# Kernel tuning notes

Measured on AMD Instinct MI355X. Metric: run time of the kernel, lower is better.

Reference implementation:

```python
import jax, jax.numpy as jnp
import numpy as np

HIDDEN = 1024
QDIM = 16
B, S = 4, 2048
EPS = 1e-8


def setup_inputs() -> dict:
    key = jax.random.key(0)
    ks = jax.random.split(key, 12)
    sc_h = 1.0 / np.sqrt(HIDDEN)
    inp = {
        "x": jax.random.normal(ks[0], (B, S, HIDDEN), dtype=jnp.float32),
        "Wq": jax.random.normal(ks[1], (HIDDEN, HIDDEN), dtype=jnp.float32) * sc_h,
        "bq": jnp.zeros((HIDDEN,), dtype=jnp.float32),
        "Wk": jax.random.normal(ks[2], (HIDDEN, HIDDEN), dtype=jnp.float32) * sc_h,
        "bk": jnp.zeros((HIDDEN,), dtype=jnp.float32),
        "Wv": jax.random.normal(ks[3], (HIDDEN, HIDDEN), dtype=jnp.float32) * sc_h,
        "bv": jnp.zeros((HIDDEN,), dtype=jnp.float32),
        "We": jax.random.normal(ks[4], (HIDDEN, QDIM), dtype=jnp.float32) * sc_h,
        "be": jnp.zeros((QDIM,), dtype=jnp.float32),
        "Wo": jax.random.normal(ks[5], (HIDDEN, HIDDEN), dtype=jnp.float32) * sc_h,
        "bo": jnp.zeros((HIDDEN,), dtype=jnp.float32),
    }
    return inp


def _quantum_embed(h, We, be):
    # Linear projection to quantum amplitude space, then normalize to a unit state.
    z = h @ We + be                     # [..., QDIM]
    nrm = jnp.sqrt(jnp.sum(z * z, axis=-1, keepdims=True) + EPS)
    return z / nrm


def reference(x, Wq, bq, Wk, bk, Wv, bv, We, be, Wo, bo):
    # Projections
    q = x @ Wq + bq                     # [B,S,H]
    k = x @ Wk + bk
    v = x @ Wv + bv
    # Quantum state embeddings (unit-normalized amplitudes)
    q_q = _quantum_embed(q, We, be)     # [B,S,QDIM]
    k_q = _quantum_embed(k, We, be)
    # Quantum fidelity similarity |<q|k>|^2, vectorized over all pairs
    ov = jnp.einsum("bqd,bkd->bqk", q_q, k_q)   # [B,S,S]
    attn = jax.nn.softmax(ov * ov, axis=-1)
    attended = jnp.einsum("bqk,bkh->bqh", attn, v)
    return attended @ Wo + bo
```

## Files before the change

kernel.cpp:

```cpp
#include <hip/hip_runtime.h>

#define H 1024
#define QD 16
#define BATCH 4
#define SEQ 2048
#define MROWS 8192
#define KCH 64

typedef __bf16 bf16x8 __attribute__((ext_vector_type(8)));
typedef __bf16 bf16x4 __attribute__((ext_vector_type(4)));
typedef float f32x4 __attribute__((ext_vector_type(4)));

__device__ __forceinline__ void async_g2l_16(const void* g, void* l) {
  __builtin_amdgcn_global_load_lds(
      (const __attribute__((address_space(1))) unsigned int*)g,
      (__attribute__((address_space(3))) unsigned int*)l, 16, 0, 0);
}

__global__ __launch_bounds__(256) void cvt_split(const float* __restrict__ src,
                                                 __bf16* __restrict__ hi,
                                                 __bf16* __restrict__ lo, int n) {
  int i = (blockIdx.x * 256 + threadIdx.x) * 4;
  if (i < n) {
    float4 f = *(const float4*)(src + i);
    bf16x4 h, l;
    h[0] = (__bf16)f.x; l[0] = (__bf16)(f.x - (float)h[0]);
    h[1] = (__bf16)f.y; l[1] = (__bf16)(f.y - (float)h[1]);
    h[2] = (__bf16)f.z; l[2] = (__bf16)(f.z - (float)h[2]);
    h[3] = (__bf16)f.w; l[3] = (__bf16)(f.w - (float)h[3]);
    *(bf16x4*)(hi + i) = h;
    *(bf16x4*)(lo + i) = l;
  }
}

__global__ __launch_bounds__(256) void transpose_cvt_f32_bf16(
    const float* __restrict__ src, __bf16* __restrict__ dst, int R, int C) {
  __shared__ float t[32][33];
  const int rb = blockIdx.y * 32, cb = blockIdx.x * 32;
  const int c = threadIdx.x & 31;
  const int r0 = threadIdx.x >> 5;
#pragma unroll
  for (int rr = r0; rr < 32; rr += 8)
    t[rr][c] = src[(long)(rb + rr) * C + cb + c];
  __syncthreads();
#pragma unroll
  for (int rr = r0; rr < 32; rr += 8)
    dst[(long)(cb + rr) * R + rb + c] = (__bf16)t[c][rr];
}

__global__ __launch_bounds__(256) void k2_cqk(const float* __restrict__ Wq,
                                              const float* __restrict__ Wk,
                                              const float* __restrict__ We,
                                              __bf16* __restrict__ Cth,
                                              __bf16* __restrict__ Ctl) {
  const int gw = blockIdx.x * 4 + (threadIdx.x >> 6);
  const int lane = threadIdx.x & 63;
  const int mat = gw & 1, k = gw >> 1;
  const float* Wrow = (mat ? Wk : Wq) + (long)k * H;
  const int col = lane & 15, q4 = lane >> 4;
  const float* wp = Wrow + q4 * 256;
  const float* wep = We + (long)q4 * 256 * QD + col;
  float acc = 0.f;
#pragma unroll 4
  for (int n0 = 0; n0 < 256; n0 += 4) {
    float4 w4 = *(const float4*)(wp + n0);
    acc += w4.x * wep[(n0 + 0) * QD];
    acc += w4.y * wep[(n0 + 1) * QD];
    acc += w4.z * wep[(n0 + 2) * QD];
    acc += w4.w * wep[(n0 + 3) * QD];
  }
  acc += __shfl_xor(acc, 16);
  acc += __shfl_xor(acc, 32);
  if (lane < 16) {
    __bf16 hi = (__bf16)acc;
    __bf16 lo = (__bf16)(acc - (float)hi);
    long idx = (long)(mat * 16 + col) * H + k;
    Cth[idx] = hi;
    Ctl[idx] = lo;
  }
}

__global__ __launch_bounds__(512) void k2b_dvec(
    const float* __restrict__ bq, const float* __restrict__ bk,
    const float* __restrict__ We, const float* __restrict__ be,
    float* __restrict__ dvec) {
  __shared__ float part[16][32];
  const int tid = threadIdx.x;
  const int j = tid & 31, p = tid >> 5;
  const int mat = j >> 4, col = j & 15;
  const float* b = mat ? bk : bq;
  float acc = 0.f;
  for (int n = p * 64; n < p * 64 + 64; ++n) acc += b[n] * We[n * QD + col];
  part[p][j] = acc;
  __syncthreads();
  if (tid < 32) {
    float sum = be[tid & 15];
    for (int p2 = 0; p2 < 16; ++p2) sum += part[p2][tid];
    dvec[tid] = sum;
  }
}

__global__ __launch_bounds__(1024) void k3_embed_mfma(
    const __bf16* __restrict__ xh, const __bf16* __restrict__ xl,
    const __bf16* __restrict__ Cth, const __bf16* __restrict__ Ctl,
    const float* __restrict__ dvec, __bf16* __restrict__ qq32,
    __bf16* __restrict__ kk32) {
  __shared__ __bf16 Ah[4][32 * 64];
  __shared__ __bf16 Al[4][32 * 64];
  __shared__ __bf16 Bh[4][32 * 64];
  __shared__ __bf16 Bl[4][32 * 64];
  const int tid = threadIdx.x;
  const int lane = tid & 63;
  const int w = tid >> 6;
  const int kb = w >> 2;
  const int w4 = w & 3;
  const int rowhalf = w4 >> 1;
  const int ntile = w4 & 1;
  const int l15 = lane & 15, quad = lane >> 4;
  const long rowBase = (long)blockIdx.x * 32;

  const int half = tid >> 8;
  const int tl = tid & 255;
  const int srow = tl >> 3;
  const int seg = tl & 7;
  const int segsw = (seg ^ (srow & 7)) * 8;
  const long gk = half * 256 + segsw;
  const __bf16* agh = xh + (rowBase + srow) * H + gk;
  const __bf16* agl = xl + (rowBase + srow) * H + gk;
  const __bf16* bgh = Cth + (long)srow * H + gk;
  const __bf16* bgl = Ctl + (long)srow * H + gk;
  __bf16* lah = &Ah[half][srow * 64 + seg * 8];
  __bf16* lal = &Al[half][srow * 64 + seg * 8];
  __bf16* lbh = &Bh[half][srow * 64 + seg * 8];
  __bf16* lbl = &Bl[half][srow * 64 + seg * 8];

  f32x4 acc;
  acc[0] = 0.f; acc[1] = 0.f; acc[2] = 0.f; acc[3] = 0.f;
  const int arow = (rowhalf * 16 + l15) * 64;
  const int brow = (ntile * 16 + l15) * 64;
  const int h7 = l15 & 7;

  for (int k0 = 0; k0 < 256; k0 += 64) {
    async_g2l_16(agh + k0, lah);
    async_g2l_16(agl + k0, lal);
    async_g2l_16(bgh + k0, lbh);
    async_g2l_16(bgl + k0, lbl);
    __syncthreads();
#pragma unroll
    for (int s = 0; s < 2; ++s) {
      const int slot = ((s * 4 + quad) ^ h7) * 8;
      bf16x8 fah = *(const bf16x8*)&Ah[kb][arow + slot];
      bf16x8 fal = *(const bf16x8*)&Al[kb][arow + slot];
      bf16x8 fbh = *(const bf16x8*)&Bh[kb][brow + slot];
      bf16x8 fbl = *(const bf16x8*)&Bl[kb][brow + slot];
      acc = __builtin_amdgcn_mfma_f32_16x16x32_bf16(fah, fbh, acc, 0, 0, 0);
      acc = __builtin_amdgcn_mfma_f32_16x16x32_bf16(fal, fbh, acc, 0, 0, 0);
      acc = __builtin_amdgcn_mfma_f32_16x16x32_bf16(fah, fbl, acc, 0, 0, 0);
    }
    __syncthreads();
  }

  if (kb > 0) ((f32x4*)&Ah[kb][0])[w4 * 64 + lane] = acc;
  __syncthreads();
  if (kb == 0) {
#pragma unroll
    for (int q = 1; q < 4; ++q) {
      f32x4 o = ((const f32x4*)&Ah[q][0])[w4 * 64 + lane];
      acc[0] += o[0]; acc[1] += o[1]; acc[2] += o[2]; acc[3] += o[3];
    }
    const float dv = dvec[ntile * 16 + l15];
    const float osc = ntile ? 1.0f : 1.20112240878f;
    __bf16* outp = ntile ? kk32 : qq32;
#pragma unroll
    for (int r = 0; r < 4; ++r) {
      float z = acc[r] + dv;
      float s2 = z * z;
      s2 += __shfl_xor(s2, 1);
      s2 += __shfl_xor(s2, 2);
      s2 += __shfl_xor(s2, 4);
      s2 += __shfl_xor(s2, 8);
      float val = z * rsqrtf(s2 + 1e-8f) * osc;
      long row = rowBase + rowhalf * 16 + quad * 4 + r;
      outp[row * 32 + l15] = (__bf16)val;
      outp[row * 32 + 16 + l15] = (__bf16)0.f;
    }
  }
}

__global__ __launch_bounds__(1024) void fused_attn(
    const __bf16* __restrict__ qq32, const __bf16* __restrict__ kk32,
    const __bf16* __restrict__ v_t, __bf16* __restrict__ attn) {
  __shared__ __bf16 Vlds[3][256 * KCH];
  __shared__ __bf16 Plds[2][128 * KCH];
  __shared__ float rsum2[128 * 2];
  const int tid = threadIdx.x;
  const int lane = tid & 63;
  const int w = tid >> 6;
  const int l15 = lane & 15, quad = lane >> 4;
  const int sq = w >> 1, sk = w & 1;
  const int wp_h = w & 3, wp_q = w >> 2;

  const int bid = blockIdx.x;
  const int xcd = bid & 7, s = bid >> 3;
  const int panel = xcd * 2 + (s >> 4);
  const int b = panel >> 2;
  const long hbase = (long)(panel & 3) * 256;
  const long qbase = (long)(s & 15) * 128;

  const bf16x8 bq = *(const bf16x8*)(qq32 +
      ((long)b * SEQ + qbase + sq * 16 + l15) * 32 + quad * 8);
  const __bf16* kkb = kk32 + ((long)b * SEQ + sk * 32 + l15) * 32 + quad * 8;

  const int vR = tid >> 3;
  const int vSL = (tid & 7) ^ (vR & 7);
  const __bf16* vg0 = v_t + (long)b * H * SEQ + (hbase + vR) * SEQ + vSL * 8;
  const __bf16* vg1 = vg0 + (long)128 * SEQ;

  f32x4 acc[2][4];
#pragma unroll
  for (int i = 0; i < 2; ++i)
#pragma unroll
    for (int j = 0; j < 4; ++j) {
      acc[i][j][0] = 0.f; acc[i][j][1] = 0.f; acc[i][j][2] = 0.f; acc[i][j][3] = 0.f;
    }
  float rsPart = 0.f;

  async_g2l_16(vg0, &Vlds[0][vR * KCH + (tid & 7) * 8]);
  async_g2l_16(vg1, &Vlds[0][(vR + 128) * KCH + (tid & 7) * 8]);
  bf16x8 ak[2];
  ak[0] = *(const bf16x8*)kkb;
  ak[1] = *(const bf16x8*)(kkb + 16 * 32);

  int vcur = 0, vnxt = 1;
  for (int t = 0; t < SEQ / KCH; ++t) {
    const int kn = ((t + 1) & (SEQ / KCH - 1)) * KCH;
    async_g2l_16(vg0 + kn, &Vlds[vnxt][vR * KCH + (tid & 7) * 8]);
    async_g2l_16(vg1 + kn, &Vlds[vnxt][(vR + 128) * KCH + (tid & 7) * 8]);

    __bf16* Pw = Plds[t & 1];
#pragma unroll
    for (int i = 0; i < 2; ++i) {
      f32x4 s2v;
      s2v[0] = 0.f; s2v[1] = 0.f; s2v[2] = 0.f; s2v[3] = 0.f;
      s2v = __builtin_amdgcn_mfma_f32_16x16x32_bf16(ak[i], bq, s2v, 0, 0, 0);
      bf16x4 pw;
      float part = 0.f;
#pragma unroll
      for (int r = 0; r < 4; ++r) {
        float wgt = exp2f(s2v[r] * s2v[r]);
        part += wgt;
        pw[r] = (__bf16)wgt;
      }
      rsPart += part;
      const int q = sq * 16 + l15;
      const int g = sk * 4 + i * 2 + (quad >> 1);
      *(bf16x4*)&Pw[q * KCH + ((g ^ (q & 7)) << 3) + (quad & 1) * 4] = pw;
    }
    ak[0] = *(const bf16x8*)(kkb + (long)kn * 32);
    ak[1] = *(const bf16x8*)(kkb + (long)(kn + 16) * 32);

    asm volatile("s_waitcnt lgkmcnt(0)" ::: "memory");
    asm volatile("s_waitcnt vmcnt(4)" ::: "memory");
    __builtin_amdgcn_sched_barrier(0);
    __builtin_amdgcn_s_barrier();

    const __bf16* Vr = Vlds[vcur];
#pragma unroll
    for (int ks = 0; ks < 2; ++ks) {
      bf16x8 ap[2], bv[4];
#pragma unroll
      for (int i = 0; i < 2; ++i) {
        const int q = wp_q * 32 + i * 16 + l15;
        ap[i] = *(const bf16x8*)&Pw[q * KCH + (((ks * 4 + quad) ^ (q & 7)) << 3)];
      }
#pragma unroll
      for (int j = 0; j < 4; ++j) {
        const int vr = wp_h * 64 + j * 16 + l15;
        bv[j] = *(const bf16x8*)&Vr[vr * KCH + (((ks * 4 + quad) ^ (vr & 7)) << 3)];
      }
#pragma unroll
      for (int i = 0; i < 2; ++i)
#pragma unroll
        for (int j = 0; j < 4; ++j)
          acc[i][j] =
              __builtin_amdgcn_mfma_f32_16x16x32_bf16(ap[i], bv[j], acc[i][j], 0, 0, 0);
    }
    const int third = 3 - vcur - vnxt;
    vcur = vnxt;
    vnxt = third;
  }

  {
    float vs = rsPart;
    vs += __shfl_xor(vs, 16);
    vs += __shfl_xor(vs, 32);
    if (lane < 16) rsum2[(sq * 16 + l15) * 2 + sk] = vs;
  }
  __syncthreads();

  float rinv[2][4];
#pragma unroll
  for (int i = 0; i < 2; ++i)
#pragma unroll
    for (int r = 0; r < 4; ++r) {
      int row = wp_q * 32 + i * 16 + quad * 4 + r;
      rinv[i][r] = 1.0f / (rsum2[row * 2] + rsum2[row * 2 + 1]);
    }

  __bf16* ob = attn + ((long)b * SEQ + qbase) * H + hbase;
#pragma unroll
  for (int i = 0; i < 2; ++i)
#pragma unroll
    for (int j = 0; j < 4; ++j) {
      const int colL = wp_h * 64 + j * 16 + l15;
#pragma unroll
      for (int r = 0; r < 4; ++r) {
        const int rowL = wp_q * 32 + i * 16 + quad * 4 + r;
        ob[(long)rowL * H + colL] = (__bf16)(acc[i][j][r] * rinv[i][r]);
      }
    }
}

template <int OUTMODE, int HASBIAS>
__global__ __launch_bounds__(256) void gemm_bt(
    const __bf16* __restrict__ A, const __bf16* __restrict__ Bt,
    void* __restrict__ Cout, const float* __restrict__ bias, int M, int N, int K) {
  __shared__ __bf16 Alds[128 * 64];
  __shared__ __bf16 Blds[128 * 64];
  const int tid = threadIdx.x;
  const int lane = tid & 63;
  const int w = tid >> 6;
  const int wm = w >> 1, wn = w & 1;
  const int l15 = lane & 15, quad = lane >> 4;

  const int flat = blockIdx.y * 8 + blockIdx.x;
  const int xcd = flat & 7, idx = flat >> 3;
  const int rowPanel = xcd * 8 + (idx >> 3);
  const int colBlk = idx & 7;
  const long rowBase = (long)rowPanel * 128;
  const long colBase = (long)colBlk * 128;

  const int srow = lane >> 3;
  const int segsw = ((lane & 7) ^ srow) * 8;

  const __bf16* ag[4];
  const __bf16* bg[4];
  __bf16* as_[4];
  __bf16* bs_[4];
#pragma unroll
  for (int j = 0; j < 4; ++j) {
    int r = j * 32 + w * 8;
    ag[j] = A + (rowBase + r + srow) * (long)K + segsw;
    bg[j] = Bt + (colBase + r + srow) * (long)K + segsw;
    as_[j] = &Alds[r * 64 + (lane & 7) * 8];
    bs_[j] = &Blds[r * 64 + (lane & 7) * 8];
  }

  f32x4 acc[4][4];
#pragma unroll
  for (int i = 0; i < 4; ++i)
#pragma unroll
    for (int j = 0; j < 4; ++j) {
      acc[i][j][0] = 0.f; acc[i][j][1] = 0.f; acc[i][j][2] = 0.f; acc[i][j][3] = 0.f;
    }

  const int h7 = l15 & 7;

  for (int k0 = 0; k0 < K; k0 += 64) {
#pragma unroll
    for (int j = 0; j < 4; ++j) {
      async_g2l_16(ag[j], as_[j]);
      async_g2l_16(bg[j], bs_[j]);
      ag[j] += 64;
      bg[j] += 64;
    }
    __syncthreads();
#pragma unroll
    for (int s = 0; s < 2; ++s) {
      const int slot = ((s * 4 + quad) ^ h7) * 8;
      bf16x8 af[4], bfv[4];
#pragma unroll
      for (int i = 0; i < 4; ++i) {
        af[i] = *(const bf16x8*)&Alds[(wm * 64 + i * 16 + l15) * 64 + slot];
        bfv[i] = *(const bf16x8*)&Blds[(wn * 64 + i * 16 + l15) * 64 + slot];
      }
#pragma unroll
      for (int i = 0; i < 4; ++i)
#pragma unroll
        for (int j = 0; j < 4; ++j)
          acc[i][j] =
              __builtin_amdgcn_mfma_f32_16x16x32_bf16(af[i], bfv[j], acc[i][j], 0, 0, 0);
    }
    __syncthreads();
  }

  const long crow0 = rowBase + wm * 64 + quad * 4;
  const long ccol0 = colBase + wn * 64 + l15;
#pragma unroll
  for (int i = 0; i < 4; ++i) {
#pragma unroll
    for (int j = 0; j < 4; ++j) {
      long col = ccol0 + j * 16;
      float bb = HASBIAS ? bias[col] : 0.f;
      if (OUTMODE == 2) {
        long row0 = crow0 + i * 16;
        int bz = (int)(row0 >> 11);
        long rb = row0 & (SEQ - 1);
        bf16x4 pv;
#pragma unroll
        for (int r = 0; r < 4; ++r) pv[r] = (__bf16)(acc[i][j][r] + bb);
        *(bf16x4*)&((__bf16*)Cout)[((long)bz * N + col) * SEQ + rb] = pv;
      } else {
#pragma unroll
        for (int r = 0; r < 4; ++r) {
          long row = crow0 + i * 16 + r;
          float val = acc[i][j][r] + bb;
          if (OUTMODE == 0)
            ((float*)Cout)[row * N + col] = val;
          else
            ((__bf16*)Cout)[row * N + col] = (__bf16)val;
        }
      }
    }
  }
}

extern "C" void kernel_launch(void* const* d_in, const int* in_sizes, int n_in,
                              void* d_out, int out_size, void* d_ws, size_t ws_size,
                              hipStream_t stream) {
  const float* x = (const float*)d_in[0];
  const float* Wq = (const float*)d_in[1];
  const float* bq = (const float*)d_in[2];
  const float* Wk = (const float*)d_in[3];
  const float* bk = (const float*)d_in[4];
  const float* Wv = (const float*)d_in[5];
  const float* bv = (const float*)d_in[6];
  const float* We = (const float*)d_in[7];
  const float* be = (const float*)d_in[8];
  const float* Wo = (const float*)d_in[9];
  const float* bo = (const float*)d_in[10];
  float* out = (float*)d_out;

  char* ws = (char*)d_ws;
  size_t o = 0;
  auto alloc = [&](size_t n) {
    size_t r = o;
    o += (n + 255) & ~(size_t)255;
    return r;
  };
  __bf16* xbf = (__bf16*)(ws + alloc((size_t)MROWS * H * 2));
  __bf16* v_t = (__bf16*)(ws + alloc((size_t)MROWS * H * 2));
  __bf16* attn = (__bf16*)(ws + alloc((size_t)MROWS * H * 2));
  __bf16* Wvt = (__bf16*)(ws + alloc((size_t)H * H * 2));
  __bf16* Wot = (__bf16*)(ws + alloc((size_t)H * H * 2));
  __bf16* Cth = (__bf16*)(ws + alloc((size_t)32 * H * 2));
  __bf16* Ctl = (__bf16*)(ws + alloc((size_t)32 * H * 2));
  float* dvec = (float*)(ws + alloc(32 * 4));
  __bf16* qq32 = (__bf16*)(ws + alloc((size_t)MROWS * 32 * 2));
  __bf16* kk32 = (__bf16*)(ws + alloc((size_t)MROWS * 32 * 2));
  __bf16* xlo = attn;
  if (ws_size < o) return;

  cvt_split<<<MROWS * H / 1024, 256, 0, stream>>>(x, xbf, xlo, MROWS * H);
  transpose_cvt_f32_bf16<<<dim3(32, 32), 256, 0, stream>>>(Wv, Wvt, H, H);
  transpose_cvt_f32_bf16<<<dim3(32, 32), 256, 0, stream>>>(Wo, Wot, H, H);
  k2_cqk<<<512, 256, 0, stream>>>(Wq, Wk, We, Cth, Ctl);
  k2b_dvec<<<1, 512, 0, stream>>>(bq, bk, We, be, dvec);
  k3_embed_mfma<<<MROWS / 32, 1024, 0, stream>>>(xbf, xlo, Cth, Ctl, dvec, qq32, kk32);
  gemm_bt<2, 1><<<dim3(8, 64), 256, 0, stream>>>(xbf, Wvt, v_t, bv, MROWS, H, H);
  fused_attn<<<256, 1024, 0, stream>>>(qq32, kk32, v_t, attn);
  gemm_bt<0, 1><<<dim3(8, 64), 256, 0, stream>>>(attn, Wot, out, bo, MROWS, H, H);
}
```

Before: 235.1 us.

## Software-pipeline attention loop: interleave next-tile score MFMAs with PV MFMAs

```diff
diff --git a/kernel.cpp b/kernel.cpp
--- a/kernel.cpp
+++ b/kernel.cpp
@@ -6,6 +6,7 @@
 #define SEQ 2048
 #define MROWS 8192
 #define KCH 64
+#define NT (SEQ / KCH)
 
 typedef __bf16 bf16x8 __attribute__((ext_vector_type(8)));
 typedef __bf16 bf16x4 __attribute__((ext_vector_type(4)));
@@ -215,6 +216,30 @@
   const int vSL = (tid & 7) ^ (vR & 7);
   const __bf16* vg0 = v_t + (long)b * H * SEQ + (hbase + vR) * SEQ + vSL * 8;
   const __bf16* vg1 = vg0 + (long)128 * SEQ;
+  const int vD0 = vR * KCH + (tid & 7) * 8;
+  const int vD1 = (vR + 128) * KCH + (tid & 7) * 8;
+
+  const int qrow = sq * 16 + l15;
+  int pwOff[2];
+#pragma unroll
+  for (int i = 0; i < 2; ++i) {
+    const int g = sk * 4 + i * 2 + (quad >> 1);
+    pwOff[i] = qrow * KCH + ((g ^ (qrow & 7)) << 3) + (quad & 1) * 4;
+  }
+  int apOff[2][2], bvOff[2][4];
+#pragma unroll
+  for (int ks = 0; ks < 2; ++ks) {
+#pragma unroll
+    for (int i = 0; i < 2; ++i) {
+      const int q = wp_q * 32 + i * 16 + l15;
+      apOff[ks][i] = q * KCH + (((ks * 4 + quad) ^ (q & 7)) << 3);
+    }
+#pragma unroll
+    for (int j = 0; j < 4; ++j) {
+      const int vr = wp_h * 64 + j * 16 + l15;
+      bvOff[ks][j] = vr * KCH + (((ks * 4 + quad) ^ (vr & 7)) << 3);
+    }
+  }
 
   f32x4 acc[2][4];
 #pragma unroll
@@ -224,71 +249,88 @@
       acc[i][j][0] = 0.f; acc[i][j][1] = 0.f; acc[i][j][2] = 0.f; acc[i][j][3] = 0.f;
     }
   float rsPart = 0.f;
-
-  async_g2l_16(vg0, &Vlds[0][vR * KCH + (tid & 7) * 8]);
-  async_g2l_16(vg1, &Vlds[0][(vR + 128) * KCH + (tid & 7) * 8]);
   bf16x8 ak[2];
+
+#define S_HALF(I, PDST)                                                       \
+  {                                                                           \
+    f32x4 sv;                                                                 \
+    sv[0] = 0.f; sv[1] = 0.f; sv[2] = 0.f; sv[3] = 0.f;                       \
+    sv = __builtin_amdgcn_mfma_f32_16x16x32_bf16(ak[I], bq, sv, 0, 0, 0);     \
+    bf16x4 pw;                                                                \
+    float w0 = exp2f(sv[0] * sv[0]);                                          \
+    float w1 = exp2f(sv[1] * sv[1]);                                          \
+    float w2 = exp2f(sv[2] * sv[2]);                                          \
+    float w3 = exp2f(sv[3] * sv[3]);                                          \
+    pw[0] = (__bf16)w0; pw[1] = (__bf16)w1;                                   \
+    pw[2] = (__bf16)w2; pw[3] = (__bf16)w3;                                   \
+    rsPart += (w0 + w1) + (w2 + w3);                                          \
+    *(bf16x4*)&(PDST)[pwOff[I]] = pw;                                         \
+  }
+
+#define ATTN_BODY(T, DOS)                                                     \
+  {                                                                           \
+    asm volatile("s_waitcnt lgkmcnt(0)" ::: "memory");                        \
+    asm volatile("s_waitcnt vmcnt(6)" ::: "memory");                          \
+    __builtin_amdgcn_sched_barrier(0);                                        \
+    __builtin_amdgcn_s_barrier();                                             \
+    const __bf16* Vr = Vlds[(T) % 3];                                         \
+    const __bf16* Pr = Plds[(T) & 1];                                         \
+    __bf16* Pw2 = Plds[((T) + 1) & 1];                                        \
+    const int kn2 = (((T) + 2) & (NT - 1)) * KCH;                             \
+    if (DOS) {                                                                \
+      __bf16* Vst = &Vlds[((T) + 2) % 3][0];                                  \
+      async_g2l_16(vg0 + kn2, &Vst[vD0]);                                     \
+      async_g2l_16(vg1 + kn2, &Vst[vD1]);                                     \
+    }                                                                         \
+    bf16x8 ap0[2], bv0[4];                                                    \
+    ap0[0] = *(const bf16x8*)&Pr[apOff[0][0]];                                \
+    ap0[1] = *(const bf16x8*)&Pr[apOff[0][1]];                                \
+    bv0[0] = *(const bf16x8*)&Vr[bvOff[0][0]];                                \
+    bv0[1] = *(const bf16x8*)&Vr[bvOff[0][1]];                                \
+    bv0[2] = *(const bf16x8*)&Vr[bvOff[0][2]];                                \
+    bv0[3] = *(const bf16x8*)&Vr[bvOff[0][3]];                                \
+    if (DOS) S_HALF(0, Pw2);                                                  \
+    _Pragma("unroll") for (int i = 0; i < 2; ++i)                             \
+      _Pragma("unroll") for (int j = 0; j < 4; ++j)                           \
+        acc[i][j] = __builtin_amdgcn_mfma_f32_16x16x32_bf16(                  \
+            ap0[i], bv0[j], acc[i][j], 0, 0, 0);                              \
+    bf16x8 ap1[2], bv1[4];                                                    \
+    ap1[0] = *(const bf16x8*)&Pr[apOff[1][0]];                                \
+    ap1[1] = *(const bf16x8*)&Pr[apOff[1][1]];                                \
+    bv1[0] = *(const bf16x8*)&Vr[bvOff[1][0]];                                \
+    bv1[1] = *(const bf16x8*)&Vr[bvOff[1][1]];                                \
+    bv1[2] = *(const bf16x8*)&Vr[bvOff[1][2]];                                \
+    bv1[3] = *(const bf16x8*)&Vr[bvOff[1][3]];                                \
+    if (DOS) S_HALF(1, Pw2);                                                  \
+    _Pragma("unroll") for (int i = 0; i < 2; ++i)                             \
+      _Pragma("unroll") for (int j = 0; j < 4; ++j)                           \
+        acc[i][j] = __builtin_amdgcn_mfma_f32_16x16x32_bf16(                  \
+            ap1[i], bv1[j], acc[i][j], 0, 0, 0);                              \
+    if (DOS) {                                                                \
+      ak[0] = *(const bf16x8*)(kkb + (long)kn2 * 32);                         \
+      ak[1] = *(const bf16x8*)(kkb + (long)(kn2 + 16) * 32);                  \
+    }                                                                         \
+  }
+
+  async_g2l_16(vg0, &Vlds[0][vD0]);
+  async_g2l_16(vg1, &Vlds[0][vD1]);
   ak[0] = *(const bf16x8*)kkb;
   ak[1] = *(const bf16x8*)(kkb + 16 * 32);
-
-  int vcur = 0, vnxt = 1;
-  for (int t = 0; t < SEQ / KCH; ++t) {
-    const int kn = ((t + 1) & (SEQ / KCH - 1)) * KCH;
-    async_g2l_16(vg0 + kn, &Vlds[vnxt][vR * KCH + (tid & 7) * 8]);
-    async_g2l_16(vg1 + kn, &Vlds[vnxt][(vR + 128) * KCH + (tid & 7) * 8]);
-
-    __bf16* Pw = Plds[t & 1];
-#pragma unroll
-    for (int i = 0; i < 2; ++i) {
-      f32x4 s2v;
-      s2v[0] = 0.f; s2v[1] = 0.f; s2v[2] = 0.f; s2v[3] = 0.f;
-      s2v = __builtin_amdgcn_mfma_f32_16x16x32_bf16(ak[i], bq, s2v, 0, 0, 0);
-      bf16x4 pw;
-      float part = 0.f;
-#pragma unroll
-      for (int r = 0; r < 4; ++r) {
-        float wgt = exp2f(s2v[r] * s2v[r]);
-        part += wgt;
-        pw[r] = (__bf16)wgt;
-      }
-      rsPart += part;
-      const int q = sq * 16 + l15;
-      const int g = sk * 4 + i * 2 + (quad >> 1);
-      *(bf16x4*)&Pw[q * KCH + ((g ^ (q & 7)) << 3) + (quad & 1) * 4] = pw;
-    }
-    ak[0] = *(const bf16x8*)(kkb + (long)kn * 32);
-    ak[1] = *(const bf16x8*)(kkb + (long)(kn + 16) * 32);
-
-    asm volatile("s_waitcnt lgkmcnt(0)" ::: "memory");
-    asm volatile("s_waitcnt vmcnt(4)" ::: "memory");
-    __builtin_amdgcn_sched_barrier(0);
-    __builtin_amdgcn_s_barrier();
-
-    const __bf16* Vr = Vlds[vcur];
-#pragma unroll
-    for (int ks = 0; ks < 2; ++ks) {
-      bf16x8 ap[2], bv[4];
-#pragma unroll
-      for (int i = 0; i < 2; ++i) {
-        const int q = wp_q * 32 + i * 16 + l15;
-        ap[i] = *(const bf16x8*)&Pw[q * KCH + (((ks * 4 + quad) ^ (q & 7)) << 3)];
-      }
-#pragma unroll
-      for (int j = 0; j < 4; ++j) {
-        const int vr = wp_h * 64 + j * 16 + l15;
-        bv[j] = *(const bf16x8*)&Vr[vr * KCH + (((ks * 4 + quad) ^ (vr & 7)) << 3)];
-      }
-#pragma unroll
-      for (int i = 0; i < 2; ++i)
-#pragma unroll
-        for (int j = 0; j < 4; ++j)
-          acc[i][j] =
-              __builtin_amdgcn_mfma_f32_16x16x32_bf16(ap[i], bv[j], acc[i][j], 0, 0, 0);
-    }
-    const int third = 3 - vcur - vnxt;
-    vcur = vnxt;
-    vnxt = third;
-  }
+  {
+    __bf16* P0 = Plds[0];
+    S_HALF(0, P0);
+    S_HALF(1, P0);
+  }
+  ak[0] = *(const bf16x8*)(kkb + (long)KCH * 32);
+  ak[1] = *(const bf16x8*)(kkb + (long)(KCH + 16) * 32);
+  async_g2l_16(vg0 + KCH, &Vlds[1][vD0]);
+  async_g2l_16(vg1 + KCH, &Vlds[1][vD1]);
+
+  for (int t = 0; t < NT - 1; ++t) ATTN_BODY(t, 1);
+  ATTN_BODY(NT - 1, 0);
+
+#undef ATTN_BODY
+#undef S_HALF
 
   {
     float vs = rsPart;
```

Measured after the change: 245.9 us. +4.6%, slower.

## Restructure fused attention around 32x32 MFMA with register-resident probabilities

Applied to the files above, without the earlier changes.

```diff
diff --git a/kernel.cpp b/kernel.cpp
--- a/kernel.cpp
+++ b/kernel.cpp
@@ -6,15 +6,25 @@
 #define SEQ 2048
 #define MROWS 8192
 #define KCH 64
+#define NT (SEQ / KCH)
 
 typedef __bf16 bf16x8 __attribute__((ext_vector_type(8)));
 typedef __bf16 bf16x4 __attribute__((ext_vector_type(4)));
 typedef float f32x4 __attribute__((ext_vector_type(4)));
+typedef float f32x16 __attribute__((ext_vector_type(16)));
+typedef unsigned int u32;
+typedef u32 u32x4 __attribute__((ext_vector_type(4)));
 
 __device__ __forceinline__ void async_g2l_16(const void* g, void* l) {
   __builtin_amdgcn_global_load_lds(
       (const __attribute__((address_space(1))) unsigned int*)g,
       (__attribute__((address_space(3))) unsigned int*)l, 16, 0, 0);
+}
+
+__device__ __forceinline__ u32 cvt_pk_bf16(float a, float b) {
+  u32 d;
+  asm("v_cvt_pk_bf16_f32 %0, %1, %2" : "=v"(d) : "v"(a), "v"(b));
+  return d;
 }
 
 __global__ __launch_bounds__(256) void cvt_split(const float* __restrict__ src,
@@ -103,8 +113,8 @@
 __global__ __launch_bounds__(1024) void k3_embed_mfma(
     const __bf16* __restrict__ xh, const __bf16* __restrict__ xl,
     const __bf16* __restrict__ Cth, const __bf16* __restrict__ Ctl,
-    const float* __restrict__ dvec, __bf16* __restrict__ qq32,
-    __bf16* __restrict__ kk32) {
+    const float* __restrict__ dvec, __bf16* __restrict__ qq16,
+    __bf16* __restrict__ kk16) {
   __shared__ __bf16 Ah[4][32 * 64];
   __shared__ __bf16 Al[4][32 * 64];
   __shared__ __bf16 Bh[4][32 * 64];
@@ -170,7 +180,7 @@
     }
     const float dv = dvec[ntile * 16 + l15];
     const float osc = ntile ? 1.0f : 1.20112240878f;
-    __bf16* outp = ntile ? kk32 : qq32;
+    __bf16* outp = ntile ? kk16 : qq16;
 #pragma unroll
     for (int r = 0; r < 4; ++r) {
       float z = acc[r] + dv;
@@ -181,24 +191,22 @@
       s2 += __shfl_xor(s2, 8);
       float val = z * rsqrtf(s2 + 1e-8f) * osc;
       long row = rowBase + rowhalf * 16 + quad * 4 + r;
-      outp[row * 32 + l15] = (__bf16)val;
-      outp[row * 32 + 16 + l15] = (__bf16)0.f;
-    }
-  }
-}
-
-__global__ __launch_bounds__(1024) void fused_attn(
-    const __bf16* __restrict__ qq32, const __bf16* __restrict__ kk32,
+      outp[row * QD + l15] = (__bf16)val;
+    }
+  }
+}
+
+__global__ __launch_bounds__(512, 2) void fused_attn(
+    const __bf16* __restrict__ qq16, const __bf16* __restrict__ kk16,
     const __bf16* __restrict__ v_t, __bf16* __restrict__ attn) {
-  __shared__ __bf16 Vlds[3][256 * KCH];
-  __shared__ __bf16 Plds[2][128 * KCH];
-  __shared__ float rsum2[128 * 2];
+  __shared__ __bf16 Vlds[2][256 * KCH];
   const int tid = threadIdx.x;
   const int lane = tid & 63;
   const int w = tid >> 6;
-  const int l15 = lane & 15, quad = lane >> 4;
-  const int sq = w >> 1, sk = w & 1;
-  const int wp_h = w & 3, wp_q = w >> 2;
+  const int l31 = lane & 31;
+  const int lh = lane >> 5;
+  const int wq = w & 3;
+  const int wh = w >> 2;
 
   const int bid = blockIdx.x;
   const int xcd = bid & 7, s = bid >> 3;
@@ -207,117 +215,119 @@
   const long hbase = (long)(panel & 3) * 256;
   const long qbase = (long)(s & 15) * 128;
 
-  const bf16x8 bq = *(const bf16x8*)(qq32 +
-      ((long)b * SEQ + qbase + sq * 16 + l15) * 32 + quad * 8);
-  const __bf16* kkb = kk32 + ((long)b * SEQ + sk * 32 + l15) * 32 + quad * 8;
+  const bf16x8 qqf = *(const bf16x8*)(
+      qq16 + ((long)b * SEQ + qbase + wq * 32 + l31) * QD + lh * 8);
+  const __bf16* kkB = kk16 + ((long)b * SEQ + l31) * QD + lh * 8;
 
   const int vR = tid >> 3;
   const int vSL = (tid & 7) ^ (vR & 7);
-  const __bf16* vg0 = v_t + (long)b * H * SEQ + (hbase + vR) * SEQ + vSL * 8;
-  const __bf16* vg1 = vg0 + (long)128 * SEQ;
-
-  f32x4 acc[2][4];
-#pragma unroll
-  for (int i = 0; i < 2; ++i)
-#pragma unroll
-    for (int j = 0; j < 4; ++j) {
-      acc[i][j][0] = 0.f; acc[i][j][1] = 0.f; acc[i][j][2] = 0.f; acc[i][j][3] = 0.f;
-    }
-  float rsPart = 0.f;
-
-  async_g2l_16(vg0, &Vlds[0][vR * KCH + (tid & 7) * 8]);
-  async_g2l_16(vg1, &Vlds[0][(vR + 128) * KCH + (tid & 7) * 8]);
-  bf16x8 ak[2];
-  ak[0] = *(const bf16x8*)kkb;
-  ak[1] = *(const bf16x8*)(kkb + 16 * 32);
-
-  int vcur = 0, vnxt = 1;
-  for (int t = 0; t < SEQ / KCH; ++t) {
-    const int kn = ((t + 1) & (SEQ / KCH - 1)) * KCH;
-    async_g2l_16(vg0 + kn, &Vlds[vnxt][vR * KCH + (tid & 7) * 8]);
-    async_g2l_16(vg1 + kn, &Vlds[vnxt][(vR + 128) * KCH + (tid & 7) * 8]);
-
-    __bf16* Pw = Plds[t & 1];
-#pragma unroll
-    for (int i = 0; i < 2; ++i) {
-      f32x4 s2v;
-      s2v[0] = 0.f; s2v[1] = 0.f; s2v[2] = 0.f; s2v[3] = 0.f;
-      s2v = __builtin_amdgcn_mfma_f32_16x16x32_bf16(ak[i], bq, s2v, 0, 0, 0);
-      bf16x4 pw;
-      float part = 0.f;
-#pragma unroll
-      for (int r = 0; r < 4; ++r) {
-        float wgt = exp2f(s2v[r] * s2v[r]);
-        part += wgt;
-        pw[r] = (__bf16)wgt;
-      }
-      rsPart += part;
-      const int q = sq * 16 + l15;
-      const int g = sk * 4 + i * 2 + (quad >> 1);
-      *(bf16x4*)&Pw[q * KCH + ((g ^ (q & 7)) << 3) + (quad & 1) * 4] = pw;
-    }
-    ak[0] = *(const bf16x8*)(kkb + (long)kn * 32);
-    ak[1] = *(const bf16x8*)(kkb + (long)(kn + 16) * 32);
-
-    asm volatile("s_waitcnt lgkmcnt(0)" ::: "memory");
-    asm volatile("s_waitcnt vmcnt(4)" ::: "memory");
+  const __bf16* vg = v_t + (long)b * H * SEQ + (hbase + vR) * SEQ + vSL * 8;
+  const int vD = vR * KCH + (tid & 7) * 8;
+
+  int vOff[4][4];
+#pragma unroll
+  for (int ht = 0; ht < 4; ++ht) {
+    const int row = wh * 128 + ht * 32 + l31;
+#pragma unroll
+    for (int kf = 0; kf < 4; ++kf)
+      vOff[ht][kf] = row * KCH + (((kf * 2 + lh) ^ (row & 7)) << 3);
+  }
+
+  f32x16 acc[4];
+#pragma unroll
+  for (int ht = 0; ht < 4; ++ht)
+#pragma unroll
+    for (int r = 0; r < 16; ++r) acc[ht][r] = 0.f;
+  float rs = 0.f;
+  bf16x8 kkf[2];
+  u32 pfw[4][4];
+
+#define S_TILE(KT)                                                            \
+  {                                                                           \
+    f32x16 sv;                                                                \
+    _Pragma("unroll") for (int r = 0; r < 16; ++r) sv[r] = 0.f;               \
+    sv = __builtin_amdgcn_mfma_f32_32x32x16_bf16(kkf[KT], qqf, sv, 0, 0, 0);  \
+    float p[16];                                                              \
+    _Pragma("unroll") for (int r = 0; r < 16; ++r) {                          \
+      p[r] = exp2f(sv[r] * sv[r]);                                            \
+      rs += p[r];                                                             \
+    }                                                                         \
+    u32 d0 = cvt_pk_bf16(p[0], p[1]), d1 = cvt_pk_bf16(p[2], p[3]);           \
+    u32 d2 = cvt_pk_bf16(p[4], p[5]), d3 = cvt_pk_bf16(p[6], p[7]);           \
+    u32 d4 = cvt_pk_bf16(p[8], p[9]), d5 = cvt_pk_bf16(p[10], p[11]);         \
+    u32 d6 = cvt_pk_bf16(p[12], p[13]), d7 = cvt_pk_bf16(p[14], p[15]);       \
+    u32 x2 = __shfl_xor(d2, 32), x0 = __shfl_xor(d0, 32);                     \
+    u32 x3 = __shfl_xor(d3, 32), x1 = __shfl_xor(d1, 32);                     \
+    pfw[(KT)*2][0] = lh ? x2 : d0;                                            \
+    pfw[(KT)*2][1] = lh ? x3 : d1;                                            \
+    pfw[(KT)*2][2] = lh ? d2 : x0;                                            \
+    pfw[(KT)*2][3] = lh ? d3 : x1;                                            \
+    u32 x6 = __shfl_xor(d6, 32), x4 = __shfl_xor(d4, 32);                     \
+    u32 x7 = __shfl_xor(d7, 32), x5 = __shfl_xor(d5, 32);                     \
+    pfw[(KT)*2 + 1][0] = lh ? x6 : d4;                                        \
+    pfw[(KT)*2 + 1][1] = lh ? x7 : d5;                                        \
+    pfw[(KT)*2 + 1][2] = lh ? d6 : x4;                                        \
+    pfw[(KT)*2 + 1][3] = lh ? d7 : x5;                                        \
+  }
+
+#define PV_CHUNK(VRP)                                                         \
+  {                                                                           \
+    const __bf16* Vr = (VRP);                                                 \
+    _Pragma("unroll") for (int kf = 0; kf < 4; ++kf) {                        \
+      u32x4 pw = {pfw[kf][0], pfw[kf][1], pfw[kf][2], pfw[kf][3]};            \
+      bf16x8 pfr = *(bf16x8*)&pw;                                             \
+      _Pragma("unroll") for (int ht = 0; ht < 4; ++ht) {                      \
+        bf16x8 av = *(const bf16x8*)&Vr[vOff[ht][kf]];                        \
+        acc[ht] = __builtin_amdgcn_mfma_f32_32x32x16_bf16(av, pfr, acc[ht],   \
+                                                          0, 0, 0);           \
+      }                                                                       \
+    }                                                                         \
+  }
+
+#define STAGE(BUF, KN)                                                        \
+  _Pragma("unroll") for (int m = 0; m < 4; ++m)                               \
+      async_g2l_16(vg + (KN) + (long)m * 64 * SEQ,                            \
+                   &Vlds[BUF][vD + m * 64 * KCH]);
+
+  STAGE(0, 0);
+  kkf[0] = *(const bf16x8*)(kkB);
+  kkf[1] = *(const bf16x8*)(kkB + 32 * QD);
+  S_TILE(0);
+  S_TILE(1);
+  asm volatile("s_waitcnt vmcnt(0)" ::: "memory");
+
+  for (int t = 0; t < NT - 1; ++t) {
+    __builtin_amdgcn_s_barrier();
+    const long kn = (long)(t + 1) * KCH;
+    kkf[0] = *(const bf16x8*)(kkB + kn * QD);
+    kkf[1] = *(const bf16x8*)(kkB + (kn + 32) * QD);
+    STAGE((t + 1) & 1, kn);
+    PV_CHUNK(Vlds[t & 1]);
+    S_TILE(0);
+    S_TILE(1);
+    asm volatile("s_waitcnt vmcnt(0)" ::: "memory");
     __builtin_amdgcn_sched_barrier(0);
-    __builtin_amdgcn_s_barrier();
-
-    const __bf16* Vr = Vlds[vcur];
-#pragma unroll
-    for (int ks = 0; ks < 2; ++ks) {
-      bf16x8 ap[2], bv[4];
-#pragma unroll
-      for (int i = 0; i < 2; ++i) {
-        const int q = wp_q * 32 + i * 16 + l15;
-        ap[i] = *(const bf16x8*)&Pw[q * KCH + (((ks * 4 + quad) ^ (q & 7)) << 3)];
-      }
-#pragma unroll
-      for (int j = 0; j < 4; ++j) {
-        const int vr = wp_h * 64 + j * 16 + l15;
-        bv[j] = *(const bf16x8*)&Vr[vr * KCH + (((ks * 4 + quad) ^ (vr & 7)) << 3)];
-      }
-#pragma unroll
-      for (int i = 0; i < 2; ++i)
-#pragma unroll
-        for (int j = 0; j < 4; ++j)
-          acc[i][j] =
-              __builtin_amdgcn_mfma_f32_16x16x32_bf16(ap[i], bv[j], acc[i][j], 0, 0, 0);
-    }
-    const int third = 3 - vcur - vnxt;
-    vcur = vnxt;
-    vnxt = third;
-  }
-
-  {
-    float vs = rsPart;
-    vs += __shfl_xor(vs, 16);
-    vs += __shfl_xor(vs, 32);
-    if (lane < 16) rsum2[(sq * 16 + l15) * 2 + sk] = vs;
-  }
-  __syncthreads();
-
-  float rinv[2][4];
-#pragma unroll
-  for (int i = 0; i < 2; ++i)
-#pragma unroll
-    for (int r = 0; r < 4; ++r) {
-      int row = wp_q * 32 + i * 16 + quad * 4 + r;
-      rinv[i][r] = 1.0f / (rsum2[row * 2] + rsum2[row * 2 + 1]);
-    }
-
-  __bf16* ob = attn + ((long)b * SEQ + qbase) * H + hbase;
-#pragma unroll
-  for (int i = 0; i < 2; ++i)
-#pragma unroll
-    for (int j = 0; j < 4; ++j) {
-      const int colL = wp_h * 64 + j * 16 + l15;
-#pragma unroll
-      for (int r = 0; r < 4; ++r) {
-        const int rowL = wp_q * 32 + i * 16 + quad * 4 + r;
-        ob[(long)rowL * H + colL] = (__bf16)(acc[i][j][r] * rinv[i][r]);
-      }
+  }
+  __builtin_amdgcn_s_barrier();
+  PV_CHUNK(Vlds[(NT - 1) & 1]);
+
+#undef STAGE
+#undef PV_CHUNK
+#undef S_TILE
+
+  const float rtot = rs + __shfl_xor(rs, 32);
+  const float rinv = 1.0f / rtot;
+
+  __bf16* ob = attn + ((long)b * SEQ + qbase + wq * 32 + l31) * H + hbase +
+               wh * 128;
+#pragma unroll
+  for (int ht = 0; ht < 4; ++ht)
+#pragma unroll
+    for (int g = 0; g < 4; ++g) {
+      bf16x4 pv;
+#pragma unroll
+      for (int e = 0; e < 4; ++e) pv[e] = (__bf16)(acc[ht][g * 4 + e] * rinv);
+      *(bf16x4*)&ob[ht * 32 + g * 8 + lh * 4] = pv;
     }
 }
 
@@ -456,8 +466,8 @@
   __bf16* Cth = (__bf16*)(ws + alloc((size_t)32 * H * 2));
   __bf16* Ctl = (__bf16*)(ws + alloc((size_t)32 * H * 2));
   float* dvec = (float*)(ws + alloc(32 * 4));
-  __bf16* qq32 = (__bf16*)(ws + alloc((size_t)MROWS * 32 * 2));
-  __bf16* kk32 = (__bf16*)(ws + alloc((size_t)MROWS * 32 * 2));
+  __bf16* qq16 = (__bf16*)(ws + alloc((size_t)MROWS * QD * 2));
+  __bf16* kk16 = (__bf16*)(ws + alloc((size_t)MROWS * QD * 2));
   __bf16* xlo = attn;
   if (ws_size < o) return;
 
@@ -466,8 +476,8 @@
   transpose_cvt_f32_bf16<<<dim3(32, 32), 256, 0, stream>>>(Wo, Wot, H, H);
   k2_cqk<<<512, 256, 0, stream>>>(Wq, Wk, We, Cth, Ctl);
   k2b_dvec<<<1, 512, 0, stream>>>(bq, bk, We, be, dvec);
-  k3_embed_mfma<<<MROWS / 32, 1024, 0, stream>>>(xbf, xlo, Cth, Ctl, dvec, qq32, kk32);
+  k3_embed_mfma<<<MROWS / 32, 1024, 0, stream>>>(xbf, xlo, Cth, Ctl, dvec, qq16, kk16);
   gemm_bt<2, 1><<<dim3(8, 64), 256, 0, stream>>>(xbf, Wvt, v_t, bv, MROWS, H, H);
-  fused_attn<<<256, 1024, 0, stream>>>(qq32, kk32, v_t, attn);
+  fused_attn<<<256, 512, 0, stream>>>(qq16, kk16, v_t, attn);
   gemm_bt<0, 1><<<dim3(8, 64), 256, 0, stream>>>(attn, Wot, out, bo, MROWS, H, H);
 }
```

New measurement: 257.9 us. 1.1x slower.
